# Kernel tuning notes

Hardware: AMD Instinct MI355X
Metric: run time of the kernel (lower is better)

The kernel has to match this reference:

```python
import jax, jax.numpy as jnp
import numpy as np

N_NODES = 100000


def _mean_agg(x, src, dst, n_nodes):
    # mean of src-node features over in-edges of each dst node (DGL copy_u + mean)
    summed = jax.ops.segment_sum(x[src], dst, num_segments=n_nodes)  # [N, F]
    deg = jax.ops.segment_sum(jnp.ones_like(src, dtype=x.dtype), dst, num_segments=n_nodes)
    return summed / jnp.maximum(deg, 1.0)[:, None]  # nodes w/o in-edges -> 0


def _sage_conv(x, src, dst, W_self, W_neigh, b):
    # DGL SAGEConv('mean'): fc_self(h) + fc_neigh(mean_neigh(h)) + bias
    h_neigh = _mean_agg(x, src, dst, x.shape[0])
    return x @ W_self + h_neigh @ W_neigh + b


def setup_inputs() -> dict:
    key = jax.random.key(0)
    ks = jax.random.split(key, 8)
    F_IN, F_H, E = 128, 128, 1600000
    s = 1.0 / np.sqrt(F_IN)
    return {
        "x": jax.random.normal(ks[0], (N_NODES, F_IN), dtype=jnp.float32),
        "src": jax.random.randint(ks[1], (E,), 0, N_NODES, dtype=jnp.int64),
        "dst": jax.random.randint(ks[2], (E,), 0, N_NODES, dtype=jnp.int64),
        "W1_self": jax.random.normal(ks[3], (F_IN, F_H), dtype=jnp.float32) * s,
        "W1_neigh": jax.random.normal(ks[4], (F_IN, F_H), dtype=jnp.float32) * s,
        "b1": jnp.zeros((F_H,), dtype=jnp.float32),
        "W2_self": jax.random.normal(ks[5], (F_H, F_H), dtype=jnp.float32) * s,
        "W2_neigh": jax.random.normal(ks[6], (F_H, F_H), dtype=jnp.float32) * s,
        "b2": jnp.zeros((F_H,), dtype=jnp.float32),
    }


def reference(x, src, dst, W1_self, W1_neigh, b1, W2_self, W2_neigh, b2):
    h = _sage_conv(x, src, dst, W1_self, W1_neigh, b1)
    # dropout in eval mode == identity
    h = jax.nn.relu(h)
    return _sage_conv(h, src, dst, W2_self, W2_neigh, b2)
```

## Files before the change

kernel.cpp:

```cpp
#include <hip/hip_runtime.h>

#define F 128
#define NN 100000
#define NBUK 782
#define NBLK 128
#define LD 136

typedef __attribute__((ext_vector_type(8))) short short8;
typedef __attribute__((ext_vector_type(4))) float f32x4;
typedef __attribute__((ext_vector_type(4))) unsigned short us4;
typedef unsigned short ushort_t;

__device__ __forceinline__ ushort_t f2b(float f) {
    union { float f; unsigned u; } x;
    x.f = f;
    unsigned r = x.u + 0x7fffu + ((x.u >> 16) & 1u);
    return (ushort_t)(r >> 16);
}
__device__ __forceinline__ float b2f(ushort_t u) {
    union { unsigned u; float f; } x;
    x.u = ((unsigned)u) << 16;
    return x.f;
}


__global__ __launch_bounds__(256) void hist_kernel(const int* __restrict__ dst,
                                                   int* __restrict__ H,
                                                   int E, int chunk) {
    __shared__ int h[NBUK];
    for (int i = threadIdx.x; i < NBUK; i += 256) h[i] = 0;
    __syncthreads();
    const int b = blockIdx.x;
    const int s0 = b * chunk, s1 = min(E, s0 + chunk);
    for (int i = s0 + threadIdx.x; i < s1; i += 256)
        atomicAdd(&h[dst[i] >> 7], 1);
    __syncthreads();
    for (int i = threadIdx.x; i < NBUK; i += 256)
        H[b * NBUK + i] = h[i];
}

__global__ __launch_bounds__(1024) void scan2(int* __restrict__ H,
                                              int* __restrict__ boffs, int E) {
    __shared__ int tot[1024];
    const int k = threadIdx.x;
    int sum = 0;
    if (k < NBUK) {
        for (int b = 0; b < NBLK; b++) {
            const int v = H[b * NBUK + k];
            H[b * NBUK + k] = sum;
            sum += v;
        }
    }
    tot[k] = (k < NBUK) ? sum : 0;
    __syncthreads();
    for (int d = 1; d < 1024; d <<= 1) {
        const int u = (k >= d) ? tot[k - d] : 0;
        __syncthreads();
        tot[k] += u;
        __syncthreads();
    }
    if (k < NBUK) boffs[k] = tot[k] - sum;
    if (k == 0) boffs[NBUK] = E;
}

__global__ __launch_bounds__(256) void scatter2(const int* __restrict__ src,
                                                const int* __restrict__ dst,
                                                const int* __restrict__ H,
                                                const int* __restrict__ boffs,
                                                unsigned* __restrict__ pairs,
                                                int E, int chunk) {
    __shared__ int cur[NBUK];
    const int b = blockIdx.x;
    for (int i = threadIdx.x; i < NBUK; i += 256)
        cur[i] = boffs[i] + H[b * NBUK + i];
    __syncthreads();
    const int s0 = b * chunk, s1 = min(E, s0 + chunk);
    for (int i = s0 + threadIdx.x; i < s1; i += 256) {
        const int d = dst[i];
        const int p = atomicAdd(&cur[d >> 7], 1);
        pairs[p] = ((unsigned)(d & 127) << 20) | (unsigned)src[i];
    }
}

__global__ __launch_bounds__(256) void bucket_sort(const unsigned* __restrict__ pairs,
                                                   const int* __restrict__ boffs,
                                                   int* __restrict__ offs,
                                                   int* __restrict__ csr) {
    __shared__ int cnt[128], loffs[128], lcur[128];
    const int b = blockIdx.x, t = threadIdx.x;
    const int e0 = boffs[b], e1 = boffs[b + 1];
    const int node0 = b << 7;
    const int nnode = min(128, NN - node0);
    if (t < 128) cnt[t] = 0;
    __syncthreads();
    for (int i = e0 + t; i < e1; i += 256) atomicAdd(&cnt[pairs[i] >> 20], 1);
    __syncthreads();
    if (t < 128) loffs[t] = cnt[t];
    __syncthreads();
    for (int d = 1; d < 128; d <<= 1) {
        int u = (t >= d && t < 128) ? loffs[t - d] : 0;
        __syncthreads();
        if (t < 128) loffs[t] += u;
        __syncthreads();
    }
    if (t < 128) {
        const int ex = loffs[t] - cnt[t];
        lcur[t] = e0 + ex;
        if (t < nnode) offs[node0 + t] = e0 + ex;
    }
    if (b == NBUK - 1 && t == 0) offs[NN] = e1;
    __syncthreads();
    for (int i = e0 + t; i < e1; i += 256) {
        const unsigned v = pairs[i];
        const int p = atomicAdd(&lcur[v >> 20], 1);
        csr[p] = (int)(v & 0xFFFFFu);
    }
}

__global__ void cvt_kernel(const float* __restrict__ X, ushort_t* __restrict__ Y, int n4) {
    int i = blockIdx.x * blockDim.x + threadIdx.x;
    if (i < n4) {
        float4 v = ((const float4*)X)[i];
        us4 o;
        o.x = f2b(v.x); o.y = f2b(v.y); o.z = f2b(v.z); o.w = f2b(v.w);
        ((us4*)Y)[i] = o;
    }
}

__global__ __launch_bounds__(256) void wt_all(
    const float* __restrict__ Wa, const float* __restrict__ Wb,
    const float* __restrict__ Wc, const float* __restrict__ Wd,
    ushort_t* __restrict__ Oa, ushort_t* __restrict__ Ob,
    ushort_t* __restrict__ Oc, ushort_t* __restrict__ Od) {
    __shared__ float tile[32][33];
    const int m = blockIdx.x >> 4;
    const int b = blockIdx.x & 15;
    const float* W = (m == 0) ? Wa : (m == 1) ? Wb : (m == 2) ? Wc : Wd;
    ushort_t* WT = (m == 0) ? Oa : (m == 1) ? Ob : (m == 2) ? Oc : Od;
    const int by = (b >> 2) * 32;
    const int bx = (b & 3) * 32;
    const int tx = threadIdx.x & 31, ty = threadIdx.x >> 5;
    for (int i = 0; i < 32; i += 8)
        tile[ty + i][tx] = W[(by + ty + i) * F + bx + tx];
    __syncthreads();
    for (int i = 0; i < 32; i += 8)
        WT[(bx + ty + i) * F + by + tx] = f2b(tile[tx][ty + i]);
}

template <typename TOUT>
__device__ __forceinline__ void store1(TOUT* p, float v);
template <> __device__ __forceinline__ void store1<float>(float* p, float v) { *p = v; }
template <> __device__ __forceinline__ void store1<ushort_t>(ushort_t* p, float v) { *p = f2b(v); }

template <typename TOUT>
__global__ __launch_bounds__(256, 6) void sage_layer(
    const ushort_t* __restrict__ Xg,
    const int* __restrict__ offs, const int* __restrict__ csr,
    const ushort_t* __restrict__ WTs, const ushort_t* __restrict__ WTn,
    const float* __restrict__ bias,
    TOUT* __restrict__ out, int relu) {
    __shared__ __align__(16) ushort_t sX[32 * LD];
    __shared__ __align__(16) ushort_t sH[32 * LD];
    const int t = threadIdx.x;
    const int lane = t & 63;
    const int wave = t >> 6;
    const int brow0 = blockIdx.x * 32;

    {
        const ushort_t* base = Xg + (size_t)brow0 * F;
        for (int i = t; i < 32 * 16; i += 256) {
            int row = i >> 4, ch = i & 15;
            *(short8*)&sX[row * LD + ch * 8] = *(const short8*)&base[row * F + ch * 8];
        }
    }

    {
        const int slot = lane >> 4;
        const int cl = lane & 15;
        const int c8 = cl * 8;
#pragma unroll
        for (int rr = 0; rr < 2; rr++) {
            const int rloc = wave * 8 + slot * 2 + rr;
            const int row = brow0 + rloc;
            const int e0 = offs[row], e1 = offs[row + 1];
            float a0[8], a1[8], a2[8], a3[8];
#pragma unroll
            for (int j = 0; j < 8; j++) { a0[j] = a1[j] = a2[j] = a3[j] = 0.f; }
            int e = e0;
            for (; e + 3 < e1; e += 4) {
                const int s0 = csr[e], s1 = csr[e + 1], s2 = csr[e + 2], s3 = csr[e + 3];
                const short8 v0 = *(const short8*)&Xg[(size_t)s0 * F + c8];
                const short8 v1 = *(const short8*)&Xg[(size_t)s1 * F + c8];
                const short8 v2 = *(const short8*)&Xg[(size_t)s2 * F + c8];
                const short8 v3 = *(const short8*)&Xg[(size_t)s3 * F + c8];
#pragma unroll
                for (int j = 0; j < 8; j++) {
                    a0[j] += b2f((ushort_t)v0[j]);
                    a1[j] += b2f((ushort_t)v1[j]);
                    a2[j] += b2f((ushort_t)v2[j]);
                    a3[j] += b2f((ushort_t)v3[j]);
                }
            }
            for (; e < e1; e++) {
                const int s0 = csr[e];
                const short8 v0 = *(const short8*)&Xg[(size_t)s0 * F + c8];
#pragma unroll
                for (int j = 0; j < 8; j++) a0[j] += b2f((ushort_t)v0[j]);
            }
            const float inv = (e1 > e0) ? (1.0f / (float)(e1 - e0)) : 0.f;
            short8 o;
#pragma unroll
            for (int j = 0; j < 8; j++)
                o[j] = (short)f2b(((a0[j] + a1[j]) + (a2[j] + a3[j])) * inv);
            *(short8*)&sH[rloc * LD + c8] = o;
        }
    }
    __syncthreads();

    const int q = lane >> 4, nl = lane & 15;
    const int colbase = wave * 32;
    f32x4 acc00 = (f32x4)0.f, acc01 = (f32x4)0.f, acc10 = (f32x4)0.f, acc11 = (f32x4)0.f;
#pragma unroll
    for (int ks = 0; ks < 4; ks++) {
        const int ko = ks * 32 + q * 8;
        const short8 aS0 = *(const short8*)&sX[nl * LD + ko];
        const short8 aS1 = *(const short8*)&sX[(16 + nl) * LD + ko];
        const short8 aN0 = *(const short8*)&sH[nl * LD + ko];
        const short8 aN1 = *(const short8*)&sH[(16 + nl) * LD + ko];
        const size_t bo0 = (size_t)(colbase + nl) * F + ko;
        const size_t bo1 = (size_t)(colbase + 16 + nl) * F + ko;
        const short8 bS0 = *(const short8*)&WTs[bo0];
        const short8 bS1 = *(const short8*)&WTs[bo1];
        const short8 bN0 = *(const short8*)&WTn[bo0];
        const short8 bN1 = *(const short8*)&WTn[bo1];
        acc00 = __builtin_amdgcn_mfma_f32_16x16x32_bf16(aS0, bS0, acc00, 0, 0, 0);
        acc00 = __builtin_amdgcn_mfma_f32_16x16x32_bf16(aN0, bN0, acc00, 0, 0, 0);
        acc01 = __builtin_amdgcn_mfma_f32_16x16x32_bf16(aS0, bS1, acc01, 0, 0, 0);
        acc01 = __builtin_amdgcn_mfma_f32_16x16x32_bf16(aN0, bN1, acc01, 0, 0, 0);
        acc10 = __builtin_amdgcn_mfma_f32_16x16x32_bf16(aS1, bS0, acc10, 0, 0, 0);
        acc10 = __builtin_amdgcn_mfma_f32_16x16x32_bf16(aN1, bN0, acc10, 0, 0, 0);
        acc11 = __builtin_amdgcn_mfma_f32_16x16x32_bf16(aS1, bS1, acc11, 0, 0, 0);
        acc11 = __builtin_amdgcn_mfma_f32_16x16x32_bf16(aN1, bN1, acc11, 0, 0, 0);
    }

    const float b0 = bias[colbase + nl];
    const float b1 = bias[colbase + 16 + nl];
#pragma unroll
    for (int r = 0; r < 4; r++) {
        const int orow0 = brow0 + q * 4 + r;
        const int orow1 = brow0 + 16 + q * 4 + r;
        float v00 = acc00[r] + b0, v01 = acc01[r] + b1;
        float v10 = acc10[r] + b0, v11 = acc11[r] + b1;
        if (relu) {
            v00 = fmaxf(v00, 0.f); v01 = fmaxf(v01, 0.f);
            v10 = fmaxf(v10, 0.f); v11 = fmaxf(v11, 0.f);
        }
        store1<TOUT>(&out[(size_t)orow0 * F + colbase + nl], v00);
        store1<TOUT>(&out[(size_t)orow0 * F + colbase + 16 + nl], v01);
        store1<TOUT>(&out[(size_t)orow1 * F + colbase + nl], v10);
        store1<TOUT>(&out[(size_t)orow1 * F + colbase + 16 + nl], v11);
    }
}

extern "C" void kernel_launch(void* const* d_in, const int* in_sizes, int n_in,
                              void* d_out, int out_size, void* d_ws, size_t ws_size,
                              hipStream_t stream) {
    const float* x = (const float*)d_in[0];
    const int* src = (const int*)d_in[1];
    const int* dst = (const int*)d_in[2];
    const float* W1s = (const float*)d_in[3];
    const float* W1n = (const float*)d_in[4];
    const float* b1 = (const float*)d_in[5];
    const float* W2s = (const float*)d_in[6];
    const float* W2n = (const float*)d_in[7];
    const float* b2 = (const float*)d_in[8];
    float* out = (float*)d_out;

    const int E = in_sizes[1];
    const int N = NN;
    const int E4 = (E + 3) & ~3;
    const int chunk = (E + NBLK - 1) / NBLK;

    unsigned* pairs = (unsigned*)d_ws;
    int* csr = (int*)(pairs + E4);
    ushort_t* h1 = (ushort_t*)(csr + E4);
    ushort_t* WT1s = h1 + (size_t)N * F;
    ushort_t* WT1n = WT1s + F * F;
    ushort_t* WT2s = WT1n + F * F;
    ushort_t* WT2n = WT2s + F * F;
    int* offs = (int*)(WT2n + F * F);
    int* H = offs + (N + 1);
    int* boffs = H + NBLK * NBUK;
    ushort_t* xb = (ushort_t*)d_out;

    hist_kernel<<<NBLK, 256, 0, stream>>>(dst, H, E, chunk);
    scan2<<<1, 1024, 0, stream>>>(H, boffs, E);
    scatter2<<<NBLK, 256, 0, stream>>>(src, dst, H, boffs, pairs, E, chunk);
    bucket_sort<<<NBUK, 256, 0, stream>>>(pairs, boffs, offs, csr);

    cvt_kernel<<<(N * F / 4 + 255) / 256, 256, 0, stream>>>(x, xb, N * F / 4);
    wt_all<<<64, 256, 0, stream>>>(W1s, W1n, W2s, W2n, WT1s, WT1n, WT2s, WT2n);

    sage_layer<ushort_t><<<N / 32, 256, 0, stream>>>(
        xb, offs, csr, WT1s, WT1n, b1, h1, 1);
    sage_layer<float><<<N / 32, 256, 0, stream>>>(
        h1, offs, csr, WT2s, WT2n, b2, out, 0);
}
```

Measured before the change: 368.4 us.

## Fuse preprocessing kernels, hide scan under conversion, stage bf16 output via LDS

The histogram, weight transpose and half of the fp32-to-bf16 feature conversion are merged into one launch. The single-block prefix scan is merged with the other half of the conversion so the serial scan overlaps with useful work. The histogram block count is doubled and the sage_layer occupancy hint is raised from 6 to 8. Layer-1 bf16 output is staged through shared memory so global stores are coalesced 16-byte writes. Risks are extra register pressure from the higher occupancy bound and a longer serial column loop in the scan with more histogram rows.

```diff
diff --git a/kernel.cpp b/kernel.cpp
--- a/kernel.cpp
+++ b/kernel.cpp
@@ -3,8 +3,10 @@
 #define F 128
 #define NN 100000
 #define NBUK 782
-#define NBLK 128
+#define NBLK 256
 #define LD 136
+#define N4 (NN * F / 4)
+#define N4A (N4 / 2)
 
 typedef __attribute__((ext_vector_type(8))) short short8;
 typedef __attribute__((ext_vector_type(4))) float f32x4;
@@ -23,44 +25,90 @@
     return x.f;
 }
 
-
-__global__ __launch_bounds__(256) void hist_kernel(const int* __restrict__ dst,
-                                                   int* __restrict__ H,
-                                                   int E, int chunk) {
-    __shared__ int h[NBUK];
-    for (int i = threadIdx.x; i < NBUK; i += 256) h[i] = 0;
-    __syncthreads();
-    const int b = blockIdx.x;
-    const int s0 = b * chunk, s1 = min(E, s0 + chunk);
-    for (int i = s0 + threadIdx.x; i < s1; i += 256)
-        atomicAdd(&h[dst[i] >> 7], 1);
-    __syncthreads();
-    for (int i = threadIdx.x; i < NBUK; i += 256)
-        H[b * NBUK + i] = h[i];
-}
-
-__global__ __launch_bounds__(1024) void scan2(int* __restrict__ H,
-                                              int* __restrict__ boffs, int E) {
-    __shared__ int tot[1024];
-    const int k = threadIdx.x;
-    int sum = 0;
-    if (k < NBUK) {
-        for (int b = 0; b < NBLK; b++) {
-            const int v = H[b * NBUK + k];
-            H[b * NBUK + k] = sum;
-            sum += v;
-        }
-    }
-    tot[k] = (k < NBUK) ? sum : 0;
-    __syncthreads();
-    for (int d = 1; d < 1024; d <<= 1) {
-        const int u = (k >= d) ? tot[k - d] : 0;
-        __syncthreads();
-        tot[k] += u;
-        __syncthreads();
-    }
-    if (k < NBUK) boffs[k] = tot[k] - sum;
-    if (k == 0) boffs[NBUK] = E;
+__global__ __launch_bounds__(256) void k1_fused(
+    const int* __restrict__ dst, int* __restrict__ H, int E, int chunk,
+    const float* __restrict__ Wa, const float* __restrict__ Wb,
+    const float* __restrict__ Wc, const float* __restrict__ Wd,
+    ushort_t* __restrict__ Oa, ushort_t* __restrict__ Ob,
+    ushort_t* __restrict__ Oc, ushort_t* __restrict__ Od,
+    const float* __restrict__ X, ushort_t* __restrict__ Y) {
+    __shared__ union {
+        int h[NBUK];
+        float tile[32][33];
+    } u;
+    const int blk = blockIdx.x;
+    if (blk < NBLK) {
+        for (int i = threadIdx.x; i < NBUK; i += 256) u.h[i] = 0;
+        __syncthreads();
+        const int s0 = blk * chunk, s1 = min(E, s0 + chunk);
+        for (int i = s0 + threadIdx.x; i < s1; i += 256)
+            atomicAdd(&u.h[dst[i] >> 7], 1);
+        __syncthreads();
+        for (int i = threadIdx.x; i < NBUK; i += 256)
+            H[blk * NBUK + i] = u.h[i];
+    } else if (blk < NBLK + 64) {
+        const int m = (blk - NBLK) >> 4;
+        const int b = (blk - NBLK) & 15;
+        const float* W = (m == 0) ? Wa : (m == 1) ? Wb : (m == 2) ? Wc : Wd;
+        ushort_t* WT = (m == 0) ? Oa : (m == 1) ? Ob : (m == 2) ? Oc : Od;
+        const int by = (b >> 2) * 32;
+        const int bx = (b & 3) * 32;
+        const int tx = threadIdx.x & 31, ty = threadIdx.x >> 5;
+        for (int i = 0; i < 32; i += 8)
+            u.tile[ty + i][tx] = W[(by + ty + i) * F + bx + tx];
+        __syncthreads();
+        for (int i = 0; i < 32; i += 8)
+            WT[(bx + ty + i) * F + by + tx] = f2b(u.tile[tx][ty + i]);
+    } else {
+        const int i = (blk - NBLK - 64) * 256 + threadIdx.x;
+        if (i < N4A) {
+            float4 v = ((const float4*)X)[i];
+            us4 o;
+            o.x = f2b(v.x); o.y = f2b(v.y); o.z = f2b(v.z); o.w = f2b(v.w);
+            ((us4*)Y)[i] = o;
+        }
+    }
+}
+
+__global__ __launch_bounds__(1024) void k2_fused(
+    int* __restrict__ H, int* __restrict__ boffs, int E,
+    const float* __restrict__ X, ushort_t* __restrict__ Y) {
+    if (blockIdx.x == 0) {
+        __shared__ int tot[1024];
+        const int k = threadIdx.x;
+        int sum = 0;
+        if (k < NBUK) {
+#pragma unroll 1
+            for (int b = 0; b < NBLK; b += 4) {
+                const int v0 = H[(b + 0) * NBUK + k];
+                const int v1 = H[(b + 1) * NBUK + k];
+                const int v2 = H[(b + 2) * NBUK + k];
+                const int v3 = H[(b + 3) * NBUK + k];
+                H[(b + 0) * NBUK + k] = sum; sum += v0;
+                H[(b + 1) * NBUK + k] = sum; sum += v1;
+                H[(b + 2) * NBUK + k] = sum; sum += v2;
+                H[(b + 3) * NBUK + k] = sum; sum += v3;
+            }
+        }
+        tot[k] = (k < NBUK) ? sum : 0;
+        __syncthreads();
+        for (int d = 1; d < 1024; d <<= 1) {
+            const int u = (k >= d) ? tot[k - d] : 0;
+            __syncthreads();
+            tot[k] += u;
+            __syncthreads();
+        }
+        if (k < NBUK) boffs[k] = tot[k] - sum;
+        if (k == 0) boffs[NBUK] = E;
+    } else {
+        const int i = N4A + (blockIdx.x - 1) * 1024 + threadIdx.x;
+        if (i < N4) {
+            float4 v = ((const float4*)X)[i];
+            us4 o;
+            o.x = f2b(v.x); o.y = f2b(v.y); o.z = f2b(v.z); o.w = f2b(v.w);
+            ((us4*)Y)[i] = o;
+        }
+    }
 }
 
 __global__ __launch_bounds__(256) void scatter2(const int* __restrict__ src,
@@ -117,43 +165,8 @@
     }
 }
 
-__global__ void cvt_kernel(const float* __restrict__ X, ushort_t* __restrict__ Y, int n4) {
-    int i = blockIdx.x * blockDim.x + threadIdx.x;
-    if (i < n4) {
-        float4 v = ((const float4*)X)[i];
-        us4 o;
-        o.x = f2b(v.x); o.y = f2b(v.y); o.z = f2b(v.z); o.w = f2b(v.w);
-        ((us4*)Y)[i] = o;
-    }
-}
-
-__global__ __launch_bounds__(256) void wt_all(
-    const float* __restrict__ Wa, const float* __restrict__ Wb,
-    const float* __restrict__ Wc, const float* __restrict__ Wd,
-    ushort_t* __restrict__ Oa, ushort_t* __restrict__ Ob,
-    ushort_t* __restrict__ Oc, ushort_t* __restrict__ Od) {
-    __shared__ float tile[32][33];
-    const int m = blockIdx.x >> 4;
-    const int b = blockIdx.x & 15;
-    const float* W = (m == 0) ? Wa : (m == 1) ? Wb : (m == 2) ? Wc : Wd;
-    ushort_t* WT = (m == 0) ? Oa : (m == 1) ? Ob : (m == 2) ? Oc : Od;
-    const int by = (b >> 2) * 32;
-    const int bx = (b & 3) * 32;
-    const int tx = threadIdx.x & 31, ty = threadIdx.x >> 5;
-    for (int i = 0; i < 32; i += 8)
-        tile[ty + i][tx] = W[(by + ty + i) * F + bx + tx];
-    __syncthreads();
-    for (int i = 0; i < 32; i += 8)
-        WT[(bx + ty + i) * F + by + tx] = f2b(tile[tx][ty + i]);
-}
-
 template <typename TOUT>
-__device__ __forceinline__ void store1(TOUT* p, float v);
-template <> __device__ __forceinline__ void store1<float>(float* p, float v) { *p = v; }
-template <> __device__ __forceinline__ void store1<ushort_t>(ushort_t* p, float v) { *p = f2b(v); }
-
-template <typename TOUT>
-__global__ __launch_bounds__(256, 6) void sage_layer(
+__global__ __launch_bounds__(256, 8) void sage_layer(
     const ushort_t* __restrict__ Xg,
     const int* __restrict__ offs, const int* __restrict__ csr,
     const ushort_t* __restrict__ WTs, const ushort_t* __restrict__ WTn,
@@ -245,20 +258,44 @@
 
     const float b0 = bias[colbase + nl];
     const float b1 = bias[colbase + 16 + nl];
-#pragma unroll
-    for (int r = 0; r < 4; r++) {
-        const int orow0 = brow0 + q * 4 + r;
-        const int orow1 = brow0 + 16 + q * 4 + r;
-        float v00 = acc00[r] + b0, v01 = acc01[r] + b1;
-        float v10 = acc10[r] + b0, v11 = acc11[r] + b1;
-        if (relu) {
-            v00 = fmaxf(v00, 0.f); v01 = fmaxf(v01, 0.f);
-            v10 = fmaxf(v10, 0.f); v11 = fmaxf(v11, 0.f);
-        }
-        store1<TOUT>(&out[(size_t)orow0 * F + colbase + nl], v00);
-        store1<TOUT>(&out[(size_t)orow0 * F + colbase + 16 + nl], v01);
-        store1<TOUT>(&out[(size_t)orow1 * F + colbase + nl], v10);
-        store1<TOUT>(&out[(size_t)orow1 * F + colbase + 16 + nl], v11);
+    if constexpr (sizeof(TOUT) == 2) {
+        __syncthreads();
+#pragma unroll
+        for (int r = 0; r < 4; r++) {
+            const int lr0 = q * 4 + r, lr1 = 16 + q * 4 + r;
+            float v00 = acc00[r] + b0, v01 = acc01[r] + b1;
+            float v10 = acc10[r] + b0, v11 = acc11[r] + b1;
+            if (relu) {
+                v00 = fmaxf(v00, 0.f); v01 = fmaxf(v01, 0.f);
+                v10 = fmaxf(v10, 0.f); v11 = fmaxf(v11, 0.f);
+            }
+            sX[lr0 * LD + colbase + nl] = f2b(v00);
+            sX[lr0 * LD + colbase + 16 + nl] = f2b(v01);
+            sX[lr1 * LD + colbase + nl] = f2b(v10);
+            sX[lr1 * LD + colbase + 16 + nl] = f2b(v11);
+        }
+        __syncthreads();
+        TOUT* base = out + (size_t)brow0 * F;
+        for (int i = t; i < 32 * 16; i += 256) {
+            int row = i >> 4, ch = i & 15;
+            *(short8*)&base[row * F + ch * 8] = *(const short8*)&sX[row * LD + ch * 8];
+        }
+    } else {
+#pragma unroll
+        for (int r = 0; r < 4; r++) {
+            const int orow0 = brow0 + q * 4 + r;
+            const int orow1 = brow0 + 16 + q * 4 + r;
+            float v00 = acc00[r] + b0, v01 = acc01[r] + b1;
+            float v10 = acc10[r] + b0, v11 = acc11[r] + b1;
+            if (relu) {
+                v00 = fmaxf(v00, 0.f); v01 = fmaxf(v01, 0.f);
+                v10 = fmaxf(v10, 0.f); v11 = fmaxf(v11, 0.f);
+            }
+            out[(size_t)orow0 * F + colbase + nl] = v00;
+            out[(size_t)orow0 * F + colbase + 16 + nl] = v01;
+            out[(size_t)orow1 * F + colbase + nl] = v10;
+            out[(size_t)orow1 * F + colbase + 16 + nl] = v11;
+        }
     }
 }
 
@@ -293,13 +330,13 @@
     int* boffs = H + NBLK * NBUK;
     ushort_t* xb = (ushort_t*)d_out;
 
-    hist_kernel<<<NBLK, 256, 0, stream>>>(dst, H, E, chunk);
-    scan2<<<1, 1024, 0, stream>>>(H, boffs, E);
+    const int cvtA_blocks = (N4A + 255) / 256;
+    k1_fused<<<NBLK + 64 + cvtA_blocks, 256, 0, stream>>>(
+        dst, H, E, chunk, W1s, W1n, W2s, W2n, WT1s, WT1n, WT2s, WT2n, x, xb);
+    const int cvtB_blocks = (N4 - N4A + 1023) / 1024;
+    k2_fused<<<1 + cvtB_blocks, 1024, 0, stream>>>(H, boffs, E, x, xb);
     scatter2<<<NBLK, 256, 0, stream>>>(src, dst, H, boffs, pairs, E, chunk);
     bucket_sort<<<NBUK, 256, 0, stream>>>(pairs, boffs, offs, csr);
-
-    cvt_kernel<<<(N * F / 4 + 255) / 256, 256, 0, stream>>>(x, xb, N * F / 4);
-    wt_all<<<64, 256, 0, stream>>>(W1s, W1n, W2s, W2n, WT1s, WT1n, WT2s, WT2n);
 
     sage_layer<ushort_t><<<N / 32, 256, 0, stream>>>(
         xb, offs, csr, WT1s, WT1n, b1, h1, 1);
```

Measured after the change: 363.2 us. No clear change (-1.4%).
